# Performance work log

Measured on AMD Instinct MI355X. Metric: run time of the kernel, lower is better.

Reference implementation:

```python
import jax, jax.numpy as jnp
import numpy as np

D_MODEL = 2048
NUM_HEADS = 16
D_K = D_MODEL // NUM_HEADS


def setup_inputs() -> dict:
    key = jax.random.key(0)
    ks = jax.random.split(key, 9)
    s = 1.0 / np.sqrt(D_MODEL)
    x = jax.random.normal(ks[0], (4, 4096, D_MODEL), dtype=jnp.float32)
    wq = jax.random.uniform(ks[1], (D_MODEL, D_MODEL), jnp.float32, -s, s)
    bq = jax.random.uniform(ks[2], (D_MODEL,), jnp.float32, -s, s)
    wk = jax.random.uniform(ks[3], (D_MODEL, D_MODEL), jnp.float32, -s, s)
    bk = jax.random.uniform(ks[4], (D_MODEL,), jnp.float32, -s, s)
    wv = jax.random.uniform(ks[5], (D_MODEL, D_MODEL), jnp.float32, -s, s)
    bv = jax.random.uniform(ks[6], (D_MODEL,), jnp.float32, -s, s)
    wo = jax.random.uniform(ks[7], (D_MODEL, D_MODEL), jnp.float32, -s, s)
    bo = jax.random.uniform(ks[8], (D_MODEL,), jnp.float32, -s, s)
    return {"x": x, "wq": wq, "bq": bq, "wk": wk, "bk": bk,
            "wv": wv, "bv": bv, "wo": wo, "bo": bo}


def _heads(t, B, S):
    # (B, S, d_model) -> (B, H, S, d_k)
    return t.reshape(B, S, NUM_HEADS, D_K).transpose(0, 2, 1, 3)


def reference(x, wq, bq, wk, bk, wv, bv, wo, bo):
    B, S, _ = x.shape
    Q = _heads(x @ wq.T + bq, B, S)
    K = _heads(x @ wk.T + bk, B, S)
    V = _heads(x @ wv.T + bv, B, S)
    # elu(x)+1 feature map
    Q = jax.nn.elu(Q) + 1.0
    K = jax.nn.elu(K) + 1.0
    # KV: (B,H,d_k,d_k)
    KV = jnp.einsum('bhsd,bhse->bhde', K, V)
    QKV = jnp.einsum('bhsd,bhde->bhse', Q, KV)
    K_sum = jnp.sum(K, axis=-2)                      # (B,H,d_k)
    QK_sum = jnp.einsum('bhsd,bhd->bhs', Q, K_sum)   # (B,H,S)
    out = QKV / (QK_sum[..., None] + 1e-8)
    out = out.transpose(0, 2, 1, 3).reshape(B, S, D_MODEL)
    return out @ wo.T + bo
```

## Files before the change

kernel.cpp:

```cpp
#include <hip/hip_runtime.h>


#define D_MODEL 2048
#define SEQ     4096
#define BATCH   4
#define HEADS   16
#define DKH     128
#define M_TOK   16384
#define NBH     64

using frag8 = __attribute__((ext_vector_type(8))) short;
using f32x4 = __attribute__((ext_vector_type(4))) float;

typedef __attribute__((address_space(1))) const unsigned int g_u32;
typedef __attribute__((address_space(3))) unsigned int       l_u32;

__device__ __forceinline__ unsigned short f2bf(float f) {
  unsigned u = __float_as_uint(f);
  u = u + 0x7fffu + ((u >> 16) & 1u);
  return (unsigned short)(u >> 16);
}
__device__ __forceinline__ float bf2f(unsigned short h) {
  return __uint_as_float(((unsigned)h) << 16);
}

__global__ __launch_bounds__(256) void convert_f2bf_kernel(
    const float* __restrict__ in, unsigned short* __restrict__ out, int n4) {
  int i = blockIdx.x * 256 + threadIdx.x;
  if (i < n4) {
    float4 v = reinterpret_cast<const float4*>(in)[i];
    ushort4 o;
    o.x = f2bf(v.x); o.y = f2bf(v.y); o.z = f2bf(v.z); o.w = f2bf(v.w);
    reinterpret_cast<ushort4*>(out)[i] = o;
  }
}


#define ST_B(GB, LD, SLOT, KC)                                                \
  _Pragma("unroll") for (int j_ = 0; j_ < 2; ++j_)                            \
    __builtin_amdgcn_global_load_lds(                                         \
        (g_u32*)((GB) + (srow + wid * 16 + j_ * 8 + (lane >> 3)) * (LD)       \
                 + (KC) + scg * 8),                                           \
        (l_u32*)(sh + (SLOT) * 16384 + 8192 + (wid * 16 + j_ * 8) * 64),      \
        16, 0, 0);

#define ST_A(GA, LD, SP, ST, KC)                                              \
    __builtin_amdgcn_global_load_lds(                                         \
        (g_u32*)((GA) + (srow + (ST) * 32 + (wid & 3) * 8 + (lane >> 3)) * (LD) \
                 + (KC) + (wid >> 2) * 32 + scg * 8),                         \
        (l_u32*)(sh + ((SP) + (wid >> 2)) * 16384 +                           \
                 ((ST) * 32 + (wid & 3) * 8) * 64),                           \
        16, 0, 0);

#define RD_A(S0, S1, Q)                                                       \
  a0[0] = *(const frag8*)(lds + (S0) * 16384 + tA + (Q) * 2048);              \
  a0[1] = *(const frag8*)(lds + (S0) * 16384 + tA + (Q) * 2048 + 1024);       \
  a1[0] = *(const frag8*)(lds + (S1) * 16384 + tA + (Q) * 2048);              \
  a1[1] = *(const frag8*)(lds + (S1) * 16384 + tA + (Q) * 2048 + 1024);

#define RD_B(D0, D1, S0, S1)                                                  \
  _Pragma("unroll") for (int n_ = 0; n_ < 4; ++n_) {                          \
    D0[n_] = *(const frag8*)(lds + (S0) * 16384 + tB + n_ * 1024);            \
    D1[n_] = *(const frag8*)(lds + (S1) * 16384 + tB + n_ * 1024);            \
  }

#define MM8(AQ, B0, B1)                                                       \
  __builtin_amdgcn_s_setprio(1);                                              \
  _Pragma("unroll") for (int j_ = 0; j_ < 2; ++j_)                            \
  _Pragma("unroll") for (int n_ = 0; n_ < 4; ++n_)                            \
    acc[(AQ) + j_][n_] = __builtin_amdgcn_mfma_f32_16x16x32_bf16(             \
        a0[j_], B0[n_], acc[(AQ) + j_][n_], 0, 0, 0);                         \
  _Pragma("unroll") for (int j_ = 0; j_ < 2; ++j_)                            \
  _Pragma("unroll") for (int n_ = 0; n_ < 4; ++n_)                            \
    acc[(AQ) + j_][n_] = __builtin_amdgcn_mfma_f32_16x16x32_bf16(             \
        a1[j_], B1[n_], acc[(AQ) + j_][n_], 0, 0, 0);                         \
  __builtin_amdgcn_s_setprio(0);

#define BAR __builtin_amdgcn_s_barrier()
#define LG0                                                                   \
  asm volatile("s_waitcnt lgkmcnt(0)" ::: "memory");                          \
  __builtin_amdgcn_sched_barrier(0)

template <int MODE, bool XMAJOR>
__global__ __launch_bounds__(512, 2) void gemm256_nt_kernel(
    const unsigned short* __restrict__ A, long lda,
    const unsigned short* __restrict__ Bm, long ldb,
    void* __restrict__ Cv, long ldc,
    const float* __restrict__ bias, int K) {
  __shared__ unsigned short sh[65536];
  const int lane = threadIdx.x & 63, wid = threadIdx.x >> 6;
  const int wm = wid >> 2, wn = wid & 3;
  const int lr = lane & 15, lh = lane >> 4;

  const int gx = gridDim.x, gy = gridDim.y;
  const int cpx = (gx * gy) >> 3;
  const int P = blockIdx.y * gx + blockIdx.x;
  const int Lw = (P & 7) * cpx + (P >> 3);
  int bx, by;
  if (XMAJOR) { bx = Lw / gy; by = Lw - bx * gy; }
  else        { by = Lw / gx; bx = Lw - by * gx; }

  const long m0 = (long)by * 256, n0 = (long)bx * 256;
  const unsigned short* Ablk = A + m0 * lda;
  const unsigned short* Bblk = Bm + n0 * ldb;
  const int NT = K >> 6;

  const int qA = (wm * 4 + lh) ^ (lr & 7);
  const int qB = ((wn >> 1) * 4 + lh) ^ (lr & 7);
  const unsigned short* lds = sh;
  const int tA = lr * 64 + qA * 8;
  const int tB = 8192 + ((wn & 1) * 64 + lr) * 64 + qB * 8;

  const int sqd = (lane & 7) ^ (lane >> 3);
  const int scg = sqd & 3;
  const long srow = (long)((sqd >> 2) * 128);

  f32x4 acc[8][4];
#pragma unroll
  for (int m = 0; m < 8; ++m)
#pragma unroll
    for (int n = 0; n < 4; ++n) acc[m][n] = (f32x4){0.f, 0.f, 0.f, 0.f};

  frag8 a0[2], a1[2], bu0[4], bu1[4], bv0[4], bv1[4];

  ST_B(Bblk, ldb, 0, 0)
  ST_B(Bblk, ldb, 1, 32)
  ST_A(Ablk, lda, 0, 0, 0) ST_A(Ablk, lda, 0, 1, 0)
  ST_A(Ablk, lda, 0, 2, 0) ST_A(Ablk, lda, 0, 3, 0)
  if (NT > 1) {
    ST_B(Bblk, ldb, 2, 64)
    ST_B(Bblk, ldb, 3, 96)
    ST_A(Ablk, lda, 2, 0, 64) ST_A(Ablk, lda, 2, 1, 64)
  }
  asm volatile("s_waitcnt vmcnt(6)" ::: "memory");
  BAR;

  const int NI = NT >> 1;
  for (int i = 0; i < NI; ++i) {
    const int kv = i * 128 + 64, kw = i * 128 + 128, kx = i * 128 + 192;
    const bool wok = (i + 1) < NI;
    RD_A(0, 1, 0)
    RD_B(bu0, bu1, 0, 1)
    ST_A(Ablk, lda, 2, 2, kv) ST_A(Ablk, lda, 2, 3, kv)
    asm volatile("s_waitcnt lgkmcnt(8)" ::: "memory");
    BAR; LG0;
    MM8(0, bu0, bu1)
    BAR;
    RD_A(0, 1, 1)
    if (wok) { ST_B(Bblk, ldb, 0, kw) }
    BAR; LG0;
    MM8(2, bu0, bu1)
    BAR;
    RD_A(0, 1, 2)
    if (wok) { ST_B(Bblk, ldb, 1, kw + 32) }
    BAR; LG0;
    MM8(4, bu0, bu1)
    BAR;
    RD_A(0, 1, 3)
    if (wok) { ST_A(Ablk, lda, 0, 0, kw) ST_A(Ablk, lda, 0, 1, kw) }
    if (wok) asm volatile("s_waitcnt vmcnt(6)" ::: "memory");
    else     asm volatile("s_waitcnt vmcnt(0)" ::: "memory");
    BAR; LG0;
    MM8(6, bu0, bu1)
    BAR;
    RD_A(2, 3, 0)
    RD_B(bv0, bv1, 2, 3)
    if (wok) { ST_A(Ablk, lda, 0, 2, kw) ST_A(Ablk, lda, 0, 3, kw) }
    asm volatile("s_waitcnt lgkmcnt(8)" ::: "memory");
    BAR; LG0;
    MM8(0, bv0, bv1)
    BAR;
    RD_A(2, 3, 1)
    if (wok) { ST_B(Bblk, ldb, 2, kx) }
    BAR; LG0;
    MM8(2, bv0, bv1)
    BAR;
    RD_A(2, 3, 2)
    if (wok) { ST_B(Bblk, ldb, 3, kx + 32) }
    BAR; LG0;
    MM8(4, bv0, bv1)
    BAR;
    RD_A(2, 3, 3)
    if (wok) { ST_A(Ablk, lda, 2, 0, kx) ST_A(Ablk, lda, 2, 1, kx)
               asm volatile("s_waitcnt vmcnt(6)" ::: "memory"); }
    BAR; LG0;
    MM8(6, bv0, bv1)
    BAR;
  }

#pragma unroll
  for (int m = 0; m < 8; ++m)
#pragma unroll
    for (int n = 0; n < 4; ++n)
#pragma unroll
      for (int r = 0; r < 4; ++r) {
        long row = m0 + wm * 128 + (m >> 1) * 32 + (m & 1) * 16 + lh * 4 + r;
        long col = n0 + wn * 64 + n * 16 + lr;
        float v = acc[m][n][r];
        if (MODE == 0) {
          v += bias[col]; v = v > 0.f ? v + 1.f : __expf(v);
          ((unsigned short*)Cv)[row * ldc + col] = f2bf(v);
        } else if (MODE == 1) {
          v += bias[row]; v = v > 0.f ? v + 1.f : __expf(v);
          ((unsigned short*)Cv)[row * ldc + col] = f2bf(v);
        } else if (MODE == 2) {
          v += bias[row];
          ((unsigned short*)Cv)[row * ldc + col] = f2bf(v);
        } else {
          v += bias[col];
          ((float*)Cv)[row * ldc + col] = v;
        }
      }
}

__device__ __forceinline__ void stage_tile(const unsigned short* __restrict__ G,
                                           long ld, unsigned short* __restrict__ L) {
  const int w = threadIdx.x >> 6, l = threadIdx.x & 63;
#pragma unroll
  for (int r = 0; r < 4; ++r) {
    const int chunk = w * 4 + r;
    const int row = chunk * 8 + (l >> 3);
    const int col = (l & 7) * 8;
    __builtin_amdgcn_global_load_lds((g_u32*)(G + (long)row * ld + col),
                                     (l_u32*)(L + chunk * 512), 16, 0, 0);
  }
}

__device__ __forceinline__ void gemm_mainloop(const unsigned short* __restrict__ A, long lda,
                                              const unsigned short* __restrict__ B, long ldb,
                                              int K, unsigned short* lA, unsigned short* lB,
                                              f32x4 acc[4][4]) {
  const int lane = threadIdx.x & 63;
  const int wid  = threadIdx.x >> 6;
  const int wr = wid >> 1, wc = wid & 1;
  const int lr = lane & 15, lh = lane >> 4;
  for (int k0 = 0; k0 < K; k0 += 64) {
    stage_tile(A + k0, lda, lA);
    stage_tile(B + k0, ldb, lB);
    __syncthreads();
#pragma unroll
    for (int kk = 0; kk < 64; kk += 32) {
      frag8 av[4], bv[4];
#pragma unroll
      for (int m = 0; m < 4; ++m)
        av[m] = *reinterpret_cast<const frag8*>(lA + (wr * 64 + m * 16 + lr) * 64 + kk + lh * 8);
#pragma unroll
      for (int n = 0; n < 4; ++n)
        bv[n] = *reinterpret_cast<const frag8*>(lB + (wc * 64 + n * 16 + lr) * 64 + kk + lh * 8);
#pragma unroll
      for (int m = 0; m < 4; ++m)
#pragma unroll
        for (int n = 0; n < 4; ++n)
          acc[m][n] = __builtin_amdgcn_mfma_f32_16x16x32_bf16(av[m], bv[n], acc[m][n], 0, 0, 0);
    }
    __syncthreads();
  }
}

#define ACC_INIT(acc)                                   \
  _Pragma("unroll") for (int m_ = 0; m_ < 4; ++m_)      \
  _Pragma("unroll") for (int n_ = 0; n_ < 4; ++n_)      \
      acc[m_][n_] = (f32x4){0.f, 0.f, 0.f, 0.f};

__global__ __launch_bounds__(256) void kvt_partial_kernel(
    const unsigned short* __restrict__ VT, const unsigned short* __restrict__ KT,
    float* __restrict__ part) {
  __shared__ unsigned short lA[128 * 64], lB[128 * 64];
  const int z = blockIdx.x;
  const int bh = z >> 3, c = z & 7;
  const int b = bh >> 4, h = bh & 15;
  const long tOff = (long)b * SEQ + (long)c * 512;
  const unsigned short* A  = VT + (long)(h * DKH) * M_TOK + tOff;
  const unsigned short* Bm = KT + (long)(h * DKH) * M_TOK + tOff;
  f32x4 acc[4][4];
  ACC_INIT(acc);
  gemm_mainloop(A, M_TOK, Bm, M_TOK, 512, lA, lB, acc);
  const int lane = threadIdx.x & 63, wid = threadIdx.x >> 6;
  const int wr = wid >> 1, wc = wid & 1, lr = lane & 15, lh = lane >> 4;
  float* out = part + (long)z * (DKH * DKH);
#pragma unroll
  for (int m = 0; m < 4; ++m)
#pragma unroll
    for (int n = 0; n < 4; ++n)
#pragma unroll
      for (int r = 0; r < 4; ++r) {
        int row = wr * 64 + m * 16 + lh * 4 + r;
        int col = wc * 64 + n * 16 + lr;
        out[row * DKH + col] = acc[m][n][r];
      }
}

__global__ __launch_bounds__(256) void reduce_kvt_kernel(
    const float* __restrict__ part, unsigned short* __restrict__ kvt) {
  int i = blockIdx.x * 256 + threadIdx.x;
  if (i < NBH * DKH * DKH) {
    int bh = i >> 14, j = i & 16383;
    float s = 0.f;
#pragma unroll
    for (int c = 0; c < 8; ++c) s += part[(((long)bh * 8 + c) << 14) + j];
    kvt[i] = f2bf(s);
  }
}

__global__ __launch_bounds__(256) void ksum_kernel(const unsigned short* __restrict__ KT,
                                                   float* __restrict__ ksum) {
  int gr = blockIdx.x * 4 + (threadIdx.x >> 6);
  int lane = threadIdx.x & 63;
  int bh = gr >> 7, d = gr & 127;
  int b = bh >> 4, h = bh & 15;
  const unsigned short* p = KT + (long)(h * DKH + d) * M_TOK + (long)b * SEQ;
  float s = 0.f;
#pragma unroll
  for (int i = 0; i < 8; ++i) {
    uint4 v = *reinterpret_cast<const uint4*>(p + (i * 64 + lane) * 8);
    unsigned w[4] = {v.x, v.y, v.z, v.w};
#pragma unroll
    for (int j = 0; j < 4; ++j) {
      s += bf2f((unsigned short)(w[j] & 0xffff));
      s += bf2f((unsigned short)(w[j] >> 16));
    }
  }
#pragma unroll
  for (int o = 32; o > 0; o >>= 1) s += __shfl_down(s, o);
  if (lane == 0) ksum[gr] = s;
}

__global__ __launch_bounds__(256) void qsum_kernel(const unsigned short* __restrict__ Q,
                                                   const float* __restrict__ ksum,
                                                   float* __restrict__ qsum) {
  int gr = blockIdx.x * 4 + (threadIdx.x >> 6);
  int lane = threadIdx.x & 63;
  int bh = gr >> 12, s = gr & 4095;
  int b = bh >> 4, h = bh & 15;
  const unsigned short* q = Q + ((long)b * SEQ + s) * D_MODEL + h * DKH + lane * 2;
  unsigned u = *reinterpret_cast<const unsigned*>(q);
  const float* ks = ksum + bh * DKH + lane * 2;
  float sum = bf2f((unsigned short)(u & 0xffff)) * ks[0] +
              bf2f((unsigned short)(u >> 16)) * ks[1];
#pragma unroll
  for (int o = 32; o > 0; o >>= 1) sum += __shfl_down(sum, o);
  if (lane == 0) qsum[gr] = sum;
}

__global__ __launch_bounds__(256) void qkv_kernel(const unsigned short* __restrict__ Q,
                                                  const unsigned short* __restrict__ KVT,
                                                  const float* __restrict__ qsum,
                                                  unsigned short* __restrict__ attn) {
  __shared__ unsigned short lA[128 * 64], lB[128 * 64];
  const int z = blockIdx.z, b = z >> 4, h = z & 15;
  const long m0 = (long)blockIdx.y * 128;
  const unsigned short* A  = Q + ((long)b * SEQ + m0) * D_MODEL + h * DKH;
  const unsigned short* Bm = KVT + (long)z * (DKH * DKH);
  f32x4 acc[4][4];
  ACC_INIT(acc);
  gemm_mainloop(A, D_MODEL, Bm, DKH, DKH, lA, lB, acc);
  const int lane = threadIdx.x & 63, wid = threadIdx.x >> 6;
  const int wr = wid >> 1, wc = wid & 1, lr = lane & 15, lh = lane >> 4;
#pragma unroll
  for (int m = 0; m < 4; ++m)
#pragma unroll
    for (int n = 0; n < 4; ++n)
#pragma unroll
      for (int r = 0; r < 4; ++r) {
        long row = m0 + wr * 64 + m * 16 + lh * 4 + r;
        int  col = wc * 64 + n * 16 + lr;
        float dnm = qsum[(long)z * SEQ + row] + 1e-8f;
        float v = acc[m][n][r] / dnm;
        attn[((long)b * SEQ + row) * D_MODEL + h * DKH + col] = f2bf(v);
      }
}

#define OFF_XB   0L
#define OFF_WQ   (OFF_XB + (long)M_TOK * D_MODEL * 2)
#define OFF_WK   (OFF_WQ + (long)D_MODEL * D_MODEL * 2)
#define OFF_WV   (OFF_WK + (long)D_MODEL * D_MODEL * 2)
#define OFF_WO   (OFF_WV + (long)D_MODEL * D_MODEL * 2)
#define OFF_QB   (OFF_WO + (long)D_MODEL * D_MODEL * 2)
#define OFF_KT   (OFF_QB + (long)M_TOK * D_MODEL * 2)
#define OFF_VT   (OFF_KT + (long)M_TOK * D_MODEL * 2)
#define OFF_PART (OFF_VT + (long)M_TOK * D_MODEL * 2)
#define OFF_KVT  (OFF_PART + (long)512 * DKH * DKH * 4)
#define OFF_KSUM (OFF_KVT + (long)NBH * DKH * DKH * 2)
#define OFF_QSUM (OFF_KSUM + (long)NBH * DKH * 4)
#define OFF_ATTN OFF_XB

extern "C" void kernel_launch(void* const* d_in, const int* in_sizes, int n_in,
                              void* d_out, int out_size, void* d_ws, size_t ws_size,
                              hipStream_t stream) {
  const float* x  = (const float*)d_in[0];
  const float* wq = (const float*)d_in[1];
  const float* bq = (const float*)d_in[2];
  const float* wk = (const float*)d_in[3];
  const float* bk = (const float*)d_in[4];
  const float* wv = (const float*)d_in[5];
  const float* bv = (const float*)d_in[6];
  const float* wo = (const float*)d_in[7];
  const float* bo = (const float*)d_in[8];

  char* ws = (char*)d_ws;
  unsigned short* xb   = (unsigned short*)(ws + OFF_XB);
  unsigned short* wqb  = (unsigned short*)(ws + OFF_WQ);
  unsigned short* wkb  = (unsigned short*)(ws + OFF_WK);
  unsigned short* wvb  = (unsigned short*)(ws + OFF_WV);
  unsigned short* wob  = (unsigned short*)(ws + OFF_WO);
  unsigned short* Qb   = (unsigned short*)(ws + OFF_QB);
  unsigned short* KTb  = (unsigned short*)(ws + OFF_KT);
  unsigned short* VTb  = (unsigned short*)(ws + OFF_VT);
  float*          part = (float*)(ws + OFF_PART);
  unsigned short* KVTb = (unsigned short*)(ws + OFF_KVT);
  float*          ksum = (float*)(ws + OFF_KSUM);
  float*          qsum = (float*)(ws + OFF_QSUM);
  unsigned short* attn = (unsigned short*)(ws + OFF_ATTN);

  dim3 blk(256);
  dim3 blk5(512);

  convert_f2bf_kernel<<<(M_TOK * D_MODEL / 4) / 256, blk, 0, stream>>>(x, xb, M_TOK * D_MODEL / 4);
  convert_f2bf_kernel<<<(D_MODEL * D_MODEL / 4) / 256, blk, 0, stream>>>(wq, wqb, D_MODEL * D_MODEL / 4);
  convert_f2bf_kernel<<<(D_MODEL * D_MODEL / 4) / 256, blk, 0, stream>>>(wk, wkb, D_MODEL * D_MODEL / 4);
  convert_f2bf_kernel<<<(D_MODEL * D_MODEL / 4) / 256, blk, 0, stream>>>(wv, wvb, D_MODEL * D_MODEL / 4);
  convert_f2bf_kernel<<<(D_MODEL * D_MODEL / 4) / 256, blk, 0, stream>>>(wo, wob, D_MODEL * D_MODEL / 4);

  gemm256_nt_kernel<0, false><<<dim3(D_MODEL / 256, M_TOK / 256), blk5, 0, stream>>>(
      xb, D_MODEL, wqb, D_MODEL, Qb, D_MODEL, bq, D_MODEL);
  gemm256_nt_kernel<1, true><<<dim3(M_TOK / 256, D_MODEL / 256), blk5, 0, stream>>>(
      wkb, D_MODEL, xb, D_MODEL, KTb, M_TOK, bk, D_MODEL);
  gemm256_nt_kernel<2, true><<<dim3(M_TOK / 256, D_MODEL / 256), blk5, 0, stream>>>(
      wvb, D_MODEL, xb, D_MODEL, VTb, M_TOK, bv, D_MODEL);

  kvt_partial_kernel<<<512, blk, 0, stream>>>(VTb, KTb, part);
  reduce_kvt_kernel<<<(NBH * DKH * DKH) / 256, blk, 0, stream>>>(part, KVTb);

  ksum_kernel<<<(NBH * DKH) / 4, blk, 0, stream>>>(KTb, ksum);
  qsum_kernel<<<(NBH * SEQ) / 4, blk, 0, stream>>>(Qb, ksum, qsum);

  qkv_kernel<<<dim3(1, SEQ / 128, NBH), blk, 0, stream>>>(Qb, KVTb, qsum, attn);

  gemm256_nt_kernel<3, false><<<dim3(D_MODEL / 256, M_TOK / 256), blk5, 0, stream>>>(
      attn, D_MODEL, wob, D_MODEL, d_out, D_MODEL, bo, D_MODEL);
}
```

Baseline: 680.3 us.

## Fuse K-sum and Q·Ksum reductions into projection GEMM epilogues

Removes the separate ksum and qsum kernels. The K projection epilogue now reduces each row over its tokens through LDS and global atomics into ksum. The Q projection runs after K and dots its outputs with ksum, writing qsum directly. The GEMM main loop also peels its last iteration so the per-iteration prefetch guards go away. This saves re-reading K and Q from memory, at the cost of atomics, an extra LDS reduction, and a memset plus a reordered launch sequence.

After: 644.8 us. 1.06x faster.

```diff
diff --git a/kernel.cpp b/kernel.cpp
--- a/kernel.cpp
+++ b/kernel.cpp
@@ -86,7 +86,8 @@
     const unsigned short* __restrict__ A, long lda,
     const unsigned short* __restrict__ Bm, long ldb,
     void* __restrict__ Cv, long ldc,
-    const float* __restrict__ bias, int K) {
+    const float* __restrict__ bias, float* __restrict__ aux,
+    float* __restrict__ qsum, int K) {
   __shared__ unsigned short sh[65536];
   const int lane = threadIdx.x & 63, wid = threadIdx.x >> 6;
   const int wm = wid >> 2, wn = wid & 3;
@@ -127,18 +128,15 @@
   ST_B(Bblk, ldb, 1, 32)
   ST_A(Ablk, lda, 0, 0, 0) ST_A(Ablk, lda, 0, 1, 0)
   ST_A(Ablk, lda, 0, 2, 0) ST_A(Ablk, lda, 0, 3, 0)
-  if (NT > 1) {
-    ST_B(Bblk, ldb, 2, 64)
-    ST_B(Bblk, ldb, 3, 96)
-    ST_A(Ablk, lda, 2, 0, 64) ST_A(Ablk, lda, 2, 1, 64)
-  }
+  ST_B(Bblk, ldb, 2, 64)
+  ST_B(Bblk, ldb, 3, 96)
+  ST_A(Ablk, lda, 2, 0, 64) ST_A(Ablk, lda, 2, 1, 64)
   asm volatile("s_waitcnt vmcnt(6)" ::: "memory");
   BAR;
 
   const int NI = NT >> 1;
-  for (int i = 0; i < NI; ++i) {
+  for (int i = 0; i < NI - 1; ++i) {
     const int kv = i * 128 + 64, kw = i * 128 + 128, kx = i * 128 + 192;
-    const bool wok = (i + 1) < NI;
     RD_A(0, 1, 0)
     RD_B(bu0, bu1, 0, 1)
     ST_A(Ablk, lda, 2, 2, kv) ST_A(Ablk, lda, 2, 3, kv)
@@ -147,62 +145,120 @@
     MM8(0, bu0, bu1)
     BAR;
     RD_A(0, 1, 1)
-    if (wok) { ST_B(Bblk, ldb, 0, kw) }
+    ST_B(Bblk, ldb, 0, kw)
     BAR; LG0;
     MM8(2, bu0, bu1)
     BAR;
     RD_A(0, 1, 2)
-    if (wok) { ST_B(Bblk, ldb, 1, kw + 32) }
+    ST_B(Bblk, ldb, 1, kw + 32)
     BAR; LG0;
     MM8(4, bu0, bu1)
     BAR;
     RD_A(0, 1, 3)
-    if (wok) { ST_A(Ablk, lda, 0, 0, kw) ST_A(Ablk, lda, 0, 1, kw) }
-    if (wok) asm volatile("s_waitcnt vmcnt(6)" ::: "memory");
-    else     asm volatile("s_waitcnt vmcnt(0)" ::: "memory");
+    ST_A(Ablk, lda, 0, 0, kw) ST_A(Ablk, lda, 0, 1, kw)
+    asm volatile("s_waitcnt vmcnt(6)" ::: "memory");
     BAR; LG0;
     MM8(6, bu0, bu1)
     BAR;
     RD_A(2, 3, 0)
     RD_B(bv0, bv1, 2, 3)
-    if (wok) { ST_A(Ablk, lda, 0, 2, kw) ST_A(Ablk, lda, 0, 3, kw) }
+    ST_A(Ablk, lda, 0, 2, kw) ST_A(Ablk, lda, 0, 3, kw)
     asm volatile("s_waitcnt lgkmcnt(8)" ::: "memory");
     BAR; LG0;
     MM8(0, bv0, bv1)
     BAR;
     RD_A(2, 3, 1)
-    if (wok) { ST_B(Bblk, ldb, 2, kx) }
+    ST_B(Bblk, ldb, 2, kx)
     BAR; LG0;
     MM8(2, bv0, bv1)
     BAR;
     RD_A(2, 3, 2)
-    if (wok) { ST_B(Bblk, ldb, 3, kx + 32) }
+    ST_B(Bblk, ldb, 3, kx + 32)
     BAR; LG0;
     MM8(4, bv0, bv1)
     BAR;
     RD_A(2, 3, 3)
-    if (wok) { ST_A(Ablk, lda, 2, 0, kx) ST_A(Ablk, lda, 2, 1, kx)
-               asm volatile("s_waitcnt vmcnt(6)" ::: "memory"); }
+    ST_A(Ablk, lda, 2, 0, kx) ST_A(Ablk, lda, 2, 1, kx)
+    asm volatile("s_waitcnt vmcnt(6)" ::: "memory");
     BAR; LG0;
     MM8(6, bv0, bv1)
     BAR;
   }
-
+  {
+    const int kv = (NI - 1) * 128 + 64;
+    RD_A(0, 1, 0)
+    RD_B(bu0, bu1, 0, 1)
+    ST_A(Ablk, lda, 2, 2, kv) ST_A(Ablk, lda, 2, 3, kv)
+    asm volatile("s_waitcnt lgkmcnt(8)" ::: "memory");
+    BAR; LG0;
+    MM8(0, bu0, bu1)
+    BAR;
+    RD_A(0, 1, 1)
+    BAR; LG0;
+    MM8(2, bu0, bu1)
+    BAR;
+    RD_A(0, 1, 2)
+    BAR; LG0;
+    MM8(4, bu0, bu1)
+    BAR;
+    RD_A(0, 1, 3)
+    asm volatile("s_waitcnt vmcnt(0)" ::: "memory");
+    BAR; LG0;
+    MM8(6, bu0, bu1)
+    BAR;
+    RD_A(2, 3, 0)
+    RD_B(bv0, bv1, 2, 3)
+    asm volatile("s_waitcnt lgkmcnt(8)" ::: "memory");
+    BAR; LG0;
+    MM8(0, bv0, bv1)
+    BAR;
+    RD_A(2, 3, 1)
+    BAR; LG0;
+    MM8(2, bv0, bv1)
+    BAR;
+    RD_A(2, 3, 2)
+    BAR; LG0;
+    MM8(4, bv0, bv1)
+    BAR;
+    RD_A(2, 3, 3)
+    BAR; LG0;
+    MM8(6, bv0, bv1)
+    BAR;
+  }
+
+  float* red = (float*)sh;
+  if (MODE == 0 || MODE == 1) {
+    if (threadIdx.x < 512) { red[threadIdx.x] = 0.f; }
+    __syncthreads();
+  }
+  float ksv[4];
+  if (MODE == 0) {
+    const long b2048 = (m0 >> 12) * 2048;
+#pragma unroll
+    for (int n = 0; n < 4; ++n)
+      ksv[n] = aux[b2048 + n0 + wn * 64 + n * 16 + lr];
+  }
 #pragma unroll
   for (int m = 0; m < 8; ++m)
 #pragma unroll
-    for (int n = 0; n < 4; ++n)
-#pragma unroll
-      for (int r = 0; r < 4; ++r) {
-        long row = m0 + wm * 128 + (m >> 1) * 32 + (m & 1) * 16 + lh * 4 + r;
+    for (int r = 0; r < 4; ++r) {
+      const int lrow = wm * 128 + (m >> 1) * 32 + (m & 1) * 16 + lh * 4 + r;
+      const long row = m0 + lrow;
+      float part = 0.f;
+#pragma unroll
+      for (int n = 0; n < 4; ++n) {
         long col = n0 + wn * 64 + n * 16 + lr;
         float v = acc[m][n][r];
         if (MODE == 0) {
           v += bias[col]; v = v > 0.f ? v + 1.f : __expf(v);
-          ((unsigned short*)Cv)[row * ldc + col] = f2bf(v);
+          unsigned short us = f2bf(v);
+          ((unsigned short*)Cv)[row * ldc + col] = us;
+          part += bf2f(us) * ksv[n];
         } else if (MODE == 1) {
           v += bias[row]; v = v > 0.f ? v + 1.f : __expf(v);
-          ((unsigned short*)Cv)[row * ldc + col] = f2bf(v);
+          unsigned short us = f2bf(v);
+          ((unsigned short*)Cv)[row * ldc + col] = us;
+          part += bf2f(us);
         } else if (MODE == 2) {
           v += bias[row];
           ((unsigned short*)Cv)[row * ldc + col] = f2bf(v);
@@ -211,6 +267,28 @@
           ((float*)Cv)[row * ldc + col] = v;
         }
       }
+      if (MODE == 0 || MODE == 1) {
+#pragma unroll
+        for (int s = 1; s < 16; s <<= 1) part += __shfl_xor(part, s);
+        if (lr == 0) {
+          if (MODE == 0) atomicAdd(&red[lrow * 2 + (wn >> 1)], part);
+          else           atomicAdd(&red[lrow], part);
+        }
+      }
+    }
+  if (MODE == 0) {
+    __syncthreads();
+    if (threadIdx.x < 512) {
+      const int lrow = threadIdx.x >> 1, hh = threadIdx.x & 1;
+      const long grow = m0 + lrow;
+      qsum[((grow >> 12) * 16 + (n0 >> 7) + hh) * (long)SEQ + (grow & 4095)] =
+          red[threadIdx.x];
+    }
+  } else if (MODE == 1) {
+    __syncthreads();
+    if (threadIdx.x < 256)
+      atomicAdd(&aux[(n0 >> 12) * 2048 + m0 + threadIdx.x], red[threadIdx.x]);
+  }
 }
 
 __device__ __forceinline__ void stage_tile(const unsigned short* __restrict__ G,
@@ -302,46 +380,6 @@
   }
 }
 
-__global__ __launch_bounds__(256) void ksum_kernel(const unsigned short* __restrict__ KT,
-                                                   float* __restrict__ ksum) {
-  int gr = blockIdx.x * 4 + (threadIdx.x >> 6);
-  int lane = threadIdx.x & 63;
-  int bh = gr >> 7, d = gr & 127;
-  int b = bh >> 4, h = bh & 15;
-  const unsigned short* p = KT + (long)(h * DKH + d) * M_TOK + (long)b * SEQ;
-  float s = 0.f;
-#pragma unroll
-  for (int i = 0; i < 8; ++i) {
-    uint4 v = *reinterpret_cast<const uint4*>(p + (i * 64 + lane) * 8);
-    unsigned w[4] = {v.x, v.y, v.z, v.w};
-#pragma unroll
-    for (int j = 0; j < 4; ++j) {
-      s += bf2f((unsigned short)(w[j] & 0xffff));
-      s += bf2f((unsigned short)(w[j] >> 16));
-    }
-  }
-#pragma unroll
-  for (int o = 32; o > 0; o >>= 1) s += __shfl_down(s, o);
-  if (lane == 0) ksum[gr] = s;
-}
-
-__global__ __launch_bounds__(256) void qsum_kernel(const unsigned short* __restrict__ Q,
-                                                   const float* __restrict__ ksum,
-                                                   float* __restrict__ qsum) {
-  int gr = blockIdx.x * 4 + (threadIdx.x >> 6);
-  int lane = threadIdx.x & 63;
-  int bh = gr >> 12, s = gr & 4095;
-  int b = bh >> 4, h = bh & 15;
-  const unsigned short* q = Q + ((long)b * SEQ + s) * D_MODEL + h * DKH + lane * 2;
-  unsigned u = *reinterpret_cast<const unsigned*>(q);
-  const float* ks = ksum + bh * DKH + lane * 2;
-  float sum = bf2f((unsigned short)(u & 0xffff)) * ks[0] +
-              bf2f((unsigned short)(u >> 16)) * ks[1];
-#pragma unroll
-  for (int o = 32; o > 0; o >>= 1) sum += __shfl_down(sum, o);
-  if (lane == 0) qsum[gr] = sum;
-}
-
 __global__ __launch_bounds__(256) void qkv_kernel(const unsigned short* __restrict__ Q,
                                                   const unsigned short* __restrict__ KVT,
                                                   const float* __restrict__ qsum,
@@ -421,21 +459,20 @@
   convert_f2bf_kernel<<<(D_MODEL * D_MODEL / 4) / 256, blk, 0, stream>>>(wv, wvb, D_MODEL * D_MODEL / 4);
   convert_f2bf_kernel<<<(D_MODEL * D_MODEL / 4) / 256, blk, 0, stream>>>(wo, wob, D_MODEL * D_MODEL / 4);
 
+  hipMemsetAsync(ksum, 0, NBH * DKH * sizeof(float), stream);
+
+  gemm256_nt_kernel<1, true><<<dim3(M_TOK / 256, D_MODEL / 256), blk5, 0, stream>>>(
+      wkb, D_MODEL, xb, D_MODEL, KTb, M_TOK, bk, ksum, nullptr, D_MODEL);
   gemm256_nt_kernel<0, false><<<dim3(D_MODEL / 256, M_TOK / 256), blk5, 0, stream>>>(
-      xb, D_MODEL, wqb, D_MODEL, Qb, D_MODEL, bq, D_MODEL);
-  gemm256_nt_kernel<1, true><<<dim3(M_TOK / 256, D_MODEL / 256), blk5, 0, stream>>>(
-      wkb, D_MODEL, xb, D_MODEL, KTb, M_TOK, bk, D_MODEL);
+      xb, D_MODEL, wqb, D_MODEL, Qb, D_MODEL, bq, ksum, qsum, D_MODEL);
   gemm256_nt_kernel<2, true><<<dim3(M_TOK / 256, D_MODEL / 256), blk5, 0, stream>>>(
-      wvb, D_MODEL, xb, D_MODEL, VTb, M_TOK, bv, D_MODEL);
+      wvb, D_MODEL, xb, D_MODEL, VTb, M_TOK, bv, nullptr, nullptr, D_MODEL);
 
   kvt_partial_kernel<<<512, blk, 0, stream>>>(VTb, KTb, part);
   reduce_kvt_kernel<<<(NBH * DKH * DKH) / 256, blk, 0, stream>>>(part, KVTb);
 
-  ksum_kernel<<<(NBH * DKH) / 4, blk, 0, stream>>>(KTb, ksum);
-  qsum_kernel<<<(NBH * SEQ) / 4, blk, 0, stream>>>(Qb, ksum, qsum);
-
   qkv_kernel<<<dim3(1, SEQ / 128, NBH), blk, 0, stream>>>(Qb, KVTb, qsum, attn);
 
   gemm256_nt_kernel<3, false><<<dim3(D_MODEL / 256, M_TOK / 256), blk5, 0, stream>>>(
-      attn, D_MODEL, wob, D_MODEL, d_out, D_MODEL, bo, D_MODEL);
-}
+      attn, D_MODEL, wob, D_MODEL, d_out, D_MODEL, bo, nullptr, nullptr, D_MODEL);
+}
```
